# Optimization experiments

Hardware: AMD Instinct MI355X
Metric: run time of the kernel (lower is better)

The kernel has to match this reference:

```python
import jax, jax.numpy as jnp
import numpy as np

SURROGATE_SCALE = 10.0  # SuperSpike-style surrogate slope

@jax.custom_vjp
def spike_fn(v):
    # Heaviside forward (standard SNN spike function)
    return (v > 0).astype(v.dtype)

def _spike_fwd(v):
    return spike_fn(v), v

def _spike_bwd(v, g):
    surrogate = 1.0 / (SURROGATE_SCALE * jnp.abs(v) + 1.0) ** 2
    return (g * surrogate,)

spike_fn.defvjp(_spike_fwd, _spike_bwd)

def setup_inputs() -> dict:
    key = jax.random.key(0)
    B, C, T = 128, 512, 1024
    x = jax.random.normal(key, (B, C, T), dtype=jnp.float32)
    beta = jnp.asarray(0.65, dtype=jnp.float32)   # scalar leak (non-trainable default)
    Vth = jnp.ones((C,), dtype=jnp.float32)        # threshold per channel
    return {"x": x, "beta": beta, "Vth": Vth}

def reference(x, beta, Vth):
    # x: (B, C, T)  -- time_position=2, negative_mempot=True, flatten_output=False
    B, C, T = x.shape
    xs = jnp.moveaxis(x, 2, 0)  # (T, B, C): scan over time

    def step(carry, inp):
        mem, spk = carry
        rst = spk * Vth                 # einsum('ab,b->ab', spk, Vth)
        mem = mem * beta + inp - rst    # negative_mempot branch
        spk = spike_fn(mem - Vth)
        return (mem, spk), spk

    init = (jnp.zeros((B, C), x.dtype), jnp.zeros((B, C), x.dtype))
    _, spk_rec = jax.lax.scan(step, init, xs)   # (T, B, C)
    return jnp.moveaxis(spk_rec, 0, 2)          # (B, C, T)
```

## Files before the change

### kernel.cpp

```cpp
#include <hip/hip_runtime.h>


#define LIF_BC 65536
#define LIF_T  1024
#define TT     64
#define NT     (LIF_T / TT)
#define ROWS   64

__global__ __launch_bounds__(64) void lif_fwd(
    const float* __restrict__ x,
    const float* __restrict__ beta_p,
    const float* __restrict__ vth_p,
    float* __restrict__ out)
{
    __shared__ float lds[2][ROWS * TT];

    const int lane = threadIdx.x;
    const int r0   = blockIdx.x * ROWS;

    const float beta = beta_p[0];
    const float vth  = vth_p[(r0 + lane) & 511];

    const int l_row4 = lane >> 4;
    const int l_t    = lane & 15;

    float4 pf[16];

    auto issue_loads = [&](int tile) {
#pragma unroll
        for (int j = 0; j < 16; ++j) {
            const int row = 4 * j + l_row4;
            pf[j] = *(const float4*)&x[(size_t)(r0 + row) * LIF_T
                                       + (size_t)tile * TT + l_t * 4];
        }
    };

    auto write_lds = [&](float* buf) {
#pragma unroll
        for (int j = 0; j < 16; ++j) {
            const int row  = 4 * j + l_row4;
            const int slot = l_t ^ (row & 15);
            *(float4*)&buf[row * TT + slot * 4] = pf[j];
        }
    };

    float mem = 0.0f, spk = 0.0f;

    auto compute = [&](float* buf) {
        const int rbase = lane * TT;
        const int sw    = lane & 15;
#pragma unroll
        for (int g = 0; g < 16; ++g) {
            float4 v = *(float4*)&buf[rbase + (g ^ sw) * 4];
            float o0, o1, o2, o3;
            {
                float rst = __fmul_rn(spk, vth);
                mem = __fsub_rn(__fadd_rn(__fmul_rn(mem, beta), v.x), rst);
                spk = (__fsub_rn(mem, vth) > 0.0f) ? 1.0f : 0.0f;
                o0 = spk;
            }
            {
                float rst = __fmul_rn(spk, vth);
                mem = __fsub_rn(__fadd_rn(__fmul_rn(mem, beta), v.y), rst);
                spk = (__fsub_rn(mem, vth) > 0.0f) ? 1.0f : 0.0f;
                o1 = spk;
            }
            {
                float rst = __fmul_rn(spk, vth);
                mem = __fsub_rn(__fadd_rn(__fmul_rn(mem, beta), v.z), rst);
                spk = (__fsub_rn(mem, vth) > 0.0f) ? 1.0f : 0.0f;
                o2 = spk;
            }
            {
                float rst = __fmul_rn(spk, vth);
                mem = __fsub_rn(__fadd_rn(__fmul_rn(mem, beta), v.w), rst);
                spk = (__fsub_rn(mem, vth) > 0.0f) ? 1.0f : 0.0f;
                o3 = spk;
            }
            v.x = o0; v.y = o1; v.z = o2; v.w = o3;
            *(float4*)&buf[rbase + (g ^ sw) * 4] = v;
        }
    };

    auto store_tile = [&](const float* buf, int tile) {
#pragma unroll
        for (int j = 0; j < 16; ++j) {
            const int row  = 4 * j + l_row4;
            const int slot = l_t ^ (row & 15);
            float4 s = *(const float4*)&buf[row * TT + slot * 4];
            *(float4*)&out[(size_t)(r0 + row) * LIF_T
                           + (size_t)tile * TT + l_t * 4] = s;
        }
    };

    issue_loads(0);
    write_lds(lds[0]);
    issue_loads(1);

    for (int k = 0; k < NT; ++k) {
        float* cur = lds[k & 1];
        compute(cur);
        if (k + 1 < NT) write_lds(lds[(k + 1) & 1]);
        if (k + 2 < NT) issue_loads(k + 2);
        store_tile(cur, k);
    }
}

extern "C" void kernel_launch(void* const* d_in, const int* in_sizes, int n_in,
                              void* d_out, int out_size, void* d_ws, size_t ws_size,
                              hipStream_t stream) {
    const float* x    = (const float*)d_in[0];
    const float* beta = (const float*)d_in[1];
    const float* vth  = (const float*)d_in[2];
    float* out = (float*)d_out;

    dim3 grid(LIF_BC / ROWS);
    lif_fwd<<<grid, 64, 0, stream>>>(x, beta, vth, out);
}
```

Measured before the change: 523.9 us.

## Deepen load prefetch to two register tiles and use nontemporal global access

Adds a second register prefetch buffer so two tiles of global loads are in flight ahead of compute, and unrolls the tile loop by two with fixed LDS buffers. Global loads and stores switch to nontemporal builtins so streaming data bypasses cache retention. The aim is to hide more memory latency in this single-wave-per-block streaming kernel. The cost is roughly 64 more VGPRs per thread, which may lower occupancy.

```diff
diff --git a/kernel.cpp b/kernel.cpp
--- a/kernel.cpp
+++ b/kernel.cpp
@@ -7,13 +7,16 @@
 #define NT     (LIF_T / TT)
 #define ROWS   64
 
+using fvec4 = __attribute__((ext_vector_type(4))) float;
+
 __global__ __launch_bounds__(64) void lif_fwd(
     const float* __restrict__ x,
     const float* __restrict__ beta_p,
     const float* __restrict__ vth_p,
     float* __restrict__ out)
 {
-    __shared__ float lds[2][ROWS * TT];
+    __shared__ float lds0[ROWS * TT];
+    __shared__ float lds1[ROWS * TT];
 
     const int lane = threadIdx.x;
     const int r0   = blockIdx.x * ROWS;
@@ -24,23 +27,24 @@
     const int l_row4 = lane >> 4;
     const int l_t    = lane & 15;
 
-    float4 pf[16];
+    fvec4 pf0[16], pf1[16];
 
-    auto issue_loads = [&](int tile) {
+    auto issue_loads = [&](fvec4 (&pf)[16], int tile) {
 #pragma unroll
         for (int j = 0; j < 16; ++j) {
             const int row = 4 * j + l_row4;
-            pf[j] = *(const float4*)&x[(size_t)(r0 + row) * LIF_T
-                                       + (size_t)tile * TT + l_t * 4];
+            pf[j] = __builtin_nontemporal_load(
+                (const fvec4*)&x[(size_t)(r0 + row) * LIF_T
+                                 + (size_t)tile * TT + l_t * 4]);
         }
     };
 
-    auto write_lds = [&](float* buf) {
+    auto write_lds = [&](float* buf, fvec4 (&pf)[16]) {
 #pragma unroll
         for (int j = 0; j < 16; ++j) {
             const int row  = 4 * j + l_row4;
             const int slot = l_t ^ (row & 15);
-            *(float4*)&buf[row * TT + slot * 4] = pf[j];
+            *(fvec4*)&buf[row * TT + slot * 4] = pf[j];
         }
     };
 
@@ -51,34 +55,15 @@
         const int sw    = lane & 15;
 #pragma unroll
         for (int g = 0; g < 16; ++g) {
-            float4 v = *(float4*)&buf[rbase + (g ^ sw) * 4];
-            float o0, o1, o2, o3;
-            {
+            fvec4 v = *(fvec4*)&buf[rbase + (g ^ sw) * 4];
+#pragma unroll
+            for (int e = 0; e < 4; ++e) {
                 float rst = __fmul_rn(spk, vth);
-                mem = __fsub_rn(__fadd_rn(__fmul_rn(mem, beta), v.x), rst);
+                mem = __fsub_rn(__fadd_rn(__fmul_rn(mem, beta), v[e]), rst);
                 spk = (__fsub_rn(mem, vth) > 0.0f) ? 1.0f : 0.0f;
-                o0 = spk;
+                v[e] = spk;
             }
-            {
-                float rst = __fmul_rn(spk, vth);
-                mem = __fsub_rn(__fadd_rn(__fmul_rn(mem, beta), v.y), rst);
-                spk = (__fsub_rn(mem, vth) > 0.0f) ? 1.0f : 0.0f;
-                o1 = spk;
-            }
-            {
-                float rst = __fmul_rn(spk, vth);
-                mem = __fsub_rn(__fadd_rn(__fmul_rn(mem, beta), v.z), rst);
-                spk = (__fsub_rn(mem, vth) > 0.0f) ? 1.0f : 0.0f;
-                o2 = spk;
-            }
-            {
-                float rst = __fmul_rn(spk, vth);
-                mem = __fsub_rn(__fadd_rn(__fmul_rn(mem, beta), v.w), rst);
-                spk = (__fsub_rn(mem, vth) > 0.0f) ? 1.0f : 0.0f;
-                o3 = spk;
-            }
-            v.x = o0; v.y = o1; v.z = o2; v.w = o3;
-            *(float4*)&buf[rbase + (g ^ sw) * 4] = v;
+            *(fvec4*)&buf[rbase + (g ^ sw) * 4] = v;
         }
     };
 
@@ -87,22 +72,27 @@
         for (int j = 0; j < 16; ++j) {
             const int row  = 4 * j + l_row4;
             const int slot = l_t ^ (row & 15);
-            float4 s = *(const float4*)&buf[row * TT + slot * 4];
-            *(float4*)&out[(size_t)(r0 + row) * LIF_T
-                           + (size_t)tile * TT + l_t * 4] = s;
+            fvec4 s = *(const fvec4*)&buf[row * TT + slot * 4];
+            __builtin_nontemporal_store(
+                s, (fvec4*)&out[(size_t)(r0 + row) * LIF_T
+                                + (size_t)tile * TT + l_t * 4]);
         }
     };
 
-    issue_loads(0);
-    write_lds(lds[0]);
-    issue_loads(1);
+    issue_loads(pf0, 0);
+    issue_loads(pf1, 1);
+    write_lds(lds0, pf0);
+    issue_loads(pf0, 2);
 
-    for (int k = 0; k < NT; ++k) {
-        float* cur = lds[k & 1];
-        compute(cur);
-        if (k + 1 < NT) write_lds(lds[(k + 1) & 1]);
-        if (k + 2 < NT) issue_loads(k + 2);
-        store_tile(cur, k);
+    for (int k = 0; k < NT; k += 2) {
+        compute(lds0);
+        store_tile(lds0, k);
+        write_lds(lds1, pf1);
+        if (k + 3 < NT) issue_loads(pf1, k + 3);
+        compute(lds1);
+        store_tile(lds1, k + 1);
+        if (k + 2 < NT) write_lds(lds0, pf0);
+        if (k + 4 < NT) issue_loads(pf0, k + 4);
     }
 }
 
```

Result: faster. 475.1 us (-9.3%).
